# Kernel optimization log

Hardware: AMD Instinct MI355X
Metric: run time of the kernel (lower is better)

Reference implementation:

```python
import jax, jax.numpy as jnp
import numpy as np

EMBED_DIM = 768
NUM_HEADS = 12
SEGMENT_LENGTHS = (2048, 4096, 8192)
DILATION_RATES = (1, 2, 4)
LN_EPS = 1e-5


def setup_inputs() -> dict:
    rng = jax.random.key(0)
    ks = jax.random.split(rng, 6)
    B, S, E = 2, 8192, EMBED_DIM
    xavier = (2.0 / (E + E)) ** 0.5  # xavier_normal std for square fan-in/out
    return {
        "query": jax.random.normal(ks[0], (B, S, E), jnp.float32),
        "key": jax.random.normal(ks[1], (B, S, E), jnp.float32),
        "value": jax.random.normal(ks[2], (B, S, E), jnp.float32),
        "qkv_w": jax.random.normal(ks[3], (3 * E, E), jnp.float32) * xavier,
        "qkv_b": jnp.zeros((3 * E,), jnp.float32),
        "ln_w": jnp.ones((E,), jnp.float32),
        "ln_b": jnp.zeros((E,), jnp.float32),
        "out_w": jax.random.normal(ks[4], (E, E), jnp.float32) * xavier,
        "out_b": jnp.zeros((E,), jnp.float32),
    }


def _dilated_attention(q, k, v):
    # q,k,v: [b, n, h, d].  Heads are partitioned across the
    # (segment_length, dilation_rate) groups; within each group the sequence
    # is split into segments of length s and subsampled with stride r at
    # offset (i % r); plain softmax attention runs inside each dilated segment.
    b, n, h, d = q.shape
    G = len(SEGMENT_LENGTHS)
    g = h // G
    scale = 1.0 / np.sqrt(d)
    out = jnp.zeros_like(q)
    for i, (s, r) in enumerate(zip(SEGMENT_LENGTHS, DILATION_RATES)):
        off = i % r
        h0, h1 = i * g, (i + 1) * g
        m = n // s
        def seg(x):
            # [b, n, g, d] -> [b, m, s/r, g, d]
            return x[:, :, h0:h1].reshape(b, m, s, g, d)[:, :, off::r]
        qi, ki, vi = seg(q), seg(k), seg(v)
        scores = jnp.einsum("bmqgd,bmkgd->bmgqk", qi, ki) * scale
        p = jax.nn.softmax(scores, axis=-1)
        xi = jnp.einsum("bmgqk,bmkgd->bmqgd", p, vi)
        seg_out = jnp.zeros((b, m, s, g, d), q.dtype).at[:, :, off::r].set(xi)
        out = out.at[:, :, h0:h1].set(seg_out.reshape(b, n, g, d))
    return out / G


def reference(query, key, value, qkv_w, qkv_b, ln_w, ln_b, out_w, out_b):
    B, S, E = query.shape
    H = NUM_HEADS
    d = E // H
    # fused QKV projection (cross-attention path of the fused projection)
    q = (query @ qkv_w[:E].T + qkv_b[:E]).reshape(B, S, H, d)
    k = (key @ qkv_w[E:2 * E].T + qkv_b[E:2 * E]).reshape(B, S, H, d)
    v = (value @ qkv_w[2 * E:].T + qkv_b[2 * E:]).reshape(B, S, H, d)
    x = _dilated_attention(q, k, v).reshape(B, S, E)
    # MAGNETO layer norm before output projection
    mu = jnp.mean(x, axis=-1, keepdims=True)
    var = jnp.mean(jnp.square(x - mu), axis=-1, keepdims=True)
    x = (x - mu) * jax.lax.rsqrt(var + LN_EPS) * ln_w + ln_b
    return x @ out_w.T + out_b
```

## Files before the change

### kernel.cpp

```cpp
#include <hip/hip_runtime.h>
#include <hip/hip_bf16.h>
#include <math.h>

typedef __bf16 bf16_t;
typedef __bf16 bf16x8 __attribute__((ext_vector_type(8)));
typedef __bf16 bf16x4 __attribute__((ext_vector_type(4)));
typedef float f32x4 __attribute__((ext_vector_type(4)));

__device__ __forceinline__ void async_ld16(const void* g, void* l) {
  __builtin_amdgcn_global_load_lds(
      (const __attribute__((address_space(1))) unsigned int*)g,
      (__attribute__((address_space(3))) unsigned int*)l, 16, 0, 0);
}

#define BATCH 2
#define SEQ   8192
#define EMB   768
#define NHEAD 12
#define HD    64
#define TOK   (BATCH*SEQ)
#define GATH_PER_B 57344

__device__ __forceinline__ int headoff(int h) {
  int g = h >> 2;
  int base = (g == 0) ? 0 : ((g == 1) ? 32768 : 49152);
  return base + (h & 3) * (8192 >> g);
}

__device__ __forceinline__ float fast_exp2(float x) {
#if __has_builtin(__builtin_amdgcn_exp2f)
  return __builtin_amdgcn_exp2f(x);
#else
  return exp2f(x);
#endif
}

__global__ void k_cast(const float* __restrict__ in, bf16_t* __restrict__ out, int n) {
  int i = (blockIdx.x * blockDim.x + threadIdx.x) * 8;
  if (i < n) {
    float4 a = *(const float4*)(in + i);
    float4 b = *(const float4*)(in + i + 4);
    __attribute__((aligned(16))) bf16_t o[8] = {
        (bf16_t)a.x, (bf16_t)a.y, (bf16_t)a.z, (bf16_t)a.w,
        (bf16_t)b.x, (bf16_t)b.y, (bf16_t)b.z, (bf16_t)b.w};
    *(uint4*)(out + i) = *(uint4*)o;
  }
}

__global__ __launch_bounds__(256, 2)
void k_gemm_qkv(const bf16_t* __restrict__ qb, const bf16_t* __restrict__ kb,
                const bf16_t* __restrict__ vb, const bf16_t* __restrict__ wqkv,
                const float* __restrict__ qkv_bias,
                bf16_t* __restrict__ Qg, bf16_t* __restrict__ Kg, bf16_t* __restrict__ Vb) {
  const int N = 768, K = 768;
  int id = blockIdx.x;
  int wid = (id & 7) * 288 + (id >> 3);
  int z = wid / 768;
  int rem = wid - z * 768;
  int ytile = rem / 6;
  int xtile = rem - ytile * 6;
  int m0 = ytile * 128, n0 = xtile * 128;

  const bf16_t* A = (z == 0) ? qb : (z == 1) ? kb : vb;
  const bf16_t* W = wqkv + (size_t)z * N * K;
  const float* bias = qkv_bias + z * N;

  __shared__ bf16_t As[2][128][32];
  __shared__ bf16_t Bs[2][128][32];

  int tid = threadIdx.x;
  int wave = tid >> 6, lane = tid & 63;
  int q = lane >> 4, c = lane & 15;
  int wm = (wave & 1) * 64, wn = (wave >> 1) * 64;

  auto stage = [&](int k0, int bsel) {
#pragma unroll
    for (int it = 0; it < 2; ++it) {
      int ch = tid + it * 256;
      int row = ch >> 2, kb8 = (ch & 3) << 3;
      async_ld16(A + (size_t)(m0 + row) * K + k0 + kb8, &As[bsel][row][kb8]);
      async_ld16(W + (size_t)(n0 + row) * K + k0 + kb8, &Bs[bsel][row][kb8]);
    }
  };

  f32x4 acc[4][4];
#pragma unroll
  for (int i = 0; i < 4; i++)
#pragma unroll
    for (int j = 0; j < 4; j++) acc[i][j] = (f32x4){0.f, 0.f, 0.f, 0.f};

  stage(0, 0);
#pragma unroll 2
  for (int kt = 0; kt < 24; ++kt) {
    int cur = kt & 1;
    __syncthreads();
    if (kt + 1 < 24) stage((kt + 1) * 32, cur ^ 1);
    bf16x8 af[4], bfr[4];
#pragma unroll
    for (int mi = 0; mi < 4; mi++) af[mi] = *(const bf16x8*)&As[cur][wm + mi * 16 + c][q * 8];
#pragma unroll
    for (int nj = 0; nj < 4; nj++) bfr[nj] = *(const bf16x8*)&Bs[cur][wn + nj * 16 + c][q * 8];
#pragma unroll
    for (int mi = 0; mi < 4; mi++)
#pragma unroll
      for (int nj = 0; nj < 4; nj++)
        acc[mi][nj] = __builtin_amdgcn_mfma_f32_16x16x32_bf16(af[mi], bfr[nj], acc[mi][nj], 0, 0, 0);
  }

  if (z == 2) {
#pragma unroll
    for (int mi = 0; mi < 4; mi++)
#pragma unroll
      for (int nj = 0; nj < 4; nj++)
#pragma unroll
        for (int rg = 0; rg < 4; rg++) {
          int row = m0 + wm + mi * 16 + q * 4 + rg;
          int col = n0 + wn + nj * 16 + c;
          Vb[(size_t)row * N + col] = (bf16_t)(acc[mi][nj][rg] + bias[col]);
        }
  } else {
    bf16_t* dst = (z == 0) ? Qg : Kg;
    float qscale = (z == 0) ? 0.125f * 1.44269504088896f : 1.0f;
#pragma unroll
    for (int mi = 0; mi < 4; mi++)
#pragma unroll
      for (int nj = 0; nj < 4; nj++) {
        int e = n0 + wn + nj * 16 + c;
        int h = e >> 6, dim = e & 63, g2 = h >> 2;
        int rm1 = (1 << g2) - 1, sh = 11 + g2;
        int smask = (2048 << g2) - 1;
        int ho = headoff(h);
#pragma unroll
        for (int rg = 0; rg < 4; rg++) {
          int row = m0 + wm + mi * 16 + q * 4 + rg;
          float v = (acc[mi][nj][rg] + bias[e]) * qscale;
          int bb = row >> 13, p = row & 8191;
          int t = (p & smask) - g2;
          if (t >= 0 && (t & rm1) == 0) {
            int jj = (p >> sh) * 2048 + (t >> g2);
            dst[(size_t)(bb * GATH_PER_B + ho + jj) * HD + dim] = (bf16_t)v;
          }
        }
      }
  }
}

__global__ __launch_bounds__(256, 2)
void k_gemm_out(const bf16_t* __restrict__ A, const bf16_t* __restrict__ W,
                const float* __restrict__ bias, float* __restrict__ C) {
  const int N = 768, K = 768;
  int id = blockIdx.x;
  int wid = (id & 7) * 96 + (id >> 3);
  int ytile = wid / 6;
  int xtile = wid - ytile * 6;
  int m0 = ytile * 128, n0 = xtile * 128;

  __shared__ bf16_t As[2][128][32];
  __shared__ bf16_t Bs[2][128][32];

  int tid = threadIdx.x;
  int wave = tid >> 6, lane = tid & 63;
  int q = lane >> 4, c = lane & 15;
  int wm = (wave & 1) * 64, wn = (wave >> 1) * 64;

  auto stage = [&](int k0, int bsel) {
#pragma unroll
    for (int it = 0; it < 2; ++it) {
      int ch = tid + it * 256;
      int row = ch >> 2, kb8 = (ch & 3) << 3;
      async_ld16(A + (size_t)(m0 + row) * K + k0 + kb8, &As[bsel][row][kb8]);
      async_ld16(W + (size_t)(n0 + row) * K + k0 + kb8, &Bs[bsel][row][kb8]);
    }
  };

  f32x4 acc[4][4];
#pragma unroll
  for (int i = 0; i < 4; i++)
#pragma unroll
    for (int j = 0; j < 4; j++) acc[i][j] = (f32x4){0.f, 0.f, 0.f, 0.f};

  stage(0, 0);
#pragma unroll 2
  for (int kt = 0; kt < 24; ++kt) {
    int cur = kt & 1;
    __syncthreads();
    if (kt + 1 < 24) stage((kt + 1) * 32, cur ^ 1);
    bf16x8 af[4], bfr[4];
#pragma unroll
    for (int mi = 0; mi < 4; mi++) af[mi] = *(const bf16x8*)&As[cur][wm + mi * 16 + c][q * 8];
#pragma unroll
    for (int nj = 0; nj < 4; nj++) bfr[nj] = *(const bf16x8*)&Bs[cur][wn + nj * 16 + c][q * 8];
#pragma unroll
    for (int mi = 0; mi < 4; mi++)
#pragma unroll
      for (int nj = 0; nj < 4; nj++)
        acc[mi][nj] = __builtin_amdgcn_mfma_f32_16x16x32_bf16(af[mi], bfr[nj], acc[mi][nj], 0, 0, 0);
  }
#pragma unroll
  for (int mi = 0; mi < 4; mi++)
#pragma unroll
    for (int nj = 0; nj < 4; nj++)
#pragma unroll
      for (int rg = 0; rg < 4; rg++) {
        int row = m0 + wm + mi * 16 + q * 4 + rg;
        int col = n0 + wn + nj * 16 + c;
        C[(size_t)row * N + col] = acc[mi][nj][rg] + bias[col];
      }
}

__global__ __launch_bounds__(256)
void k_gather_v(const bf16_t* __restrict__ Vb, bf16_t* __restrict__ Vt) {
  int h = blockIdx.y, b = blockIdx.z;
  int g = h >> 2;
  int L = 8192 >> g;
  int jj0 = blockIdx.x * 64;
  if (jj0 >= L) return;
  int s = 2048 << g;
  int hb = b * GATH_PER_B + headoff(h);
  int tid = threadIdx.x;

  __shared__ bf16_t tile[64][72];

#pragma unroll
  for (int it = 0; it < 2; ++it) {
    int ch = tid + it * 256;
    int rowl = ch >> 3, db = (ch & 7) << 3;
    int jj = jj0 + rowl;
    int p = (jj >> 11) * s + g + ((jj & 2047) << g);
    *(uint4*)&tile[rowl][db] = *(const uint4*)(Vb + ((size_t)(b * SEQ + p)) * EMB + h * HD + db);
  }
  __syncthreads();
  int dim = tid >> 2, sub = tid & 3;
  __attribute__((aligned(16))) bf16_t tmp[16];
#pragma unroll
  for (int sl = 0; sl < 16; sl++) {
    int t = sub * 16 + sl;
    int pos = (t & 3) * 16 + (t >> 2);
    tmp[sl] = tile[pos][dim];
  }
  size_t vdst = ((size_t)hb) * HD + (size_t)dim * L + jj0 + sub * 16;
  *(uint4*)(Vt + vdst) = *(uint4*)&tmp[0];
  *(uint4*)(Vt + vdst + 8) = *(uint4*)&tmp[8];
}

__global__ __launch_bounds__(256, 2)
void k_attn(const bf16_t* __restrict__ Qg, const bf16_t* __restrict__ Kg,
            const bf16_t* __restrict__ Vt, bf16_t* __restrict__ xattn) {
  int u = blockIdx.x;
  int seg = u % 56, qt = u / 56;
  int b = seg / 28, t = seg % 28;
  int g, h, si;
  if (t < 16)      { g = 0; h = t >> 2;              si = t & 3; }
  else if (t < 24) { g = 1; h = 4 + ((t - 16) >> 1); si = (t - 16) & 1; }
  else             { g = 2; h = 8 + (t - 24);        si = 0; }
  int L = 8192 >> g, s = 2048 << g;
  int hb = b * GATH_PER_B + headoff(h);
  int jj0 = si * 2048 + qt * 128;
  int kvbase = si * 2048;

  __shared__ bf16_t Ps[128][64];
  __shared__ bf16_t Ks[2][128][64];
  __shared__ bf16_t Vs[2][64][128];

  int tid = threadIdx.x, wave = tid >> 6, lane = tid & 63;
  int q = lane >> 4, c = lane & 15;
  int cx = c & 7;
  int wm = wave * 32;

  auto stageK = [&](int kt, int bsel) {
#pragma unroll
    for (int it = 0; it < 4; ++it) {
      int ch = tid + it * 256;
      int row = ch >> 3, pc = ch & 7, lc = pc ^ (row & 7);
      async_ld16(Kg + ((size_t)(hb + kvbase + kt * 128 + row)) * HD + lc * 8,
                 &Ks[bsel][0][0] + ch * 8);
    }
  };
  auto stageV = [&](int kt, int bsel) {
#pragma unroll
    for (int it = 0; it < 4; ++it) {
      int ch = tid + it * 256;
      int dim = ch >> 4, pc = ch & 15, lc = pc ^ (dim & 7);
      async_ld16(Vt + ((size_t)hb) * HD + (size_t)dim * L + kvbase + kt * 128 + lc * 8,
                 &Vs[bsel][0][0] + ch * 8);
    }
  };

  bf16_t* Qs = &Ps[0][0];
#pragma unroll
  for (int it = 0; it < 4; ++it) {
    int ch = tid + it * 256;
    int row = ch >> 3, pc = ch & 7, lc = pc ^ (row & 7);
    async_ld16(Qg + ((size_t)(hb + jj0 + row)) * HD + lc * 8, Qs + ch * 8);
  }
  stageK(0, 0);
  stageV(0, 0);
  __syncthreads();

  bf16x8 aq[2][2];
#pragma unroll
  for (int mi = 0; mi < 2; mi++)
#pragma unroll
    for (int kq = 0; kq < 2; kq++) {
      int pch = (kq * 4 + q) ^ cx;
      aq[mi][kq] = *(const bf16x8*)(Qs + (size_t)(wm + mi * 16 + c) * HD + pch * 8);
    }

  float lrow[2][4];
  f32x4 O[2][4];
#pragma unroll
  for (int mi = 0; mi < 2; mi++)
#pragma unroll
    for (int rg = 0; rg < 4; rg++) lrow[mi][rg] = 0.f;
#pragma unroll
  for (int mi = 0; mi < 2; mi++)
#pragma unroll
    for (int vd = 0; vd < 4; vd++) O[mi][vd] = (f32x4){0.f, 0.f, 0.f, 0.f};

#pragma unroll 2
  for (int kt = 0; kt < 16; ++kt) {
    int cur = kt & 1;
    if (kt < 15) {
      stageK(kt + 1, cur ^ 1);
      stageV(kt + 1, cur ^ 1);
    }

    f32x4 Sv[2][8];
#pragma unroll
    for (int mi = 0; mi < 2; mi++)
#pragma unroll
      for (int nj = 0; nj < 8; nj++) Sv[mi][nj] = (f32x4){0.f, 0.f, 0.f, 0.f};
#pragma unroll
    for (int kq = 0; kq < 2; kq++) {
      int pch = (kq * 4 + q) ^ cx;
      bf16x8 bk[8];
#pragma unroll
      for (int nj = 0; nj < 8; nj++) bk[nj] = *(const bf16x8*)&Ks[cur][nj * 16 + c][pch * 8];
#pragma unroll
      for (int mi = 0; mi < 2; mi++)
#pragma unroll
        for (int nj = 0; nj < 8; nj++)
          Sv[mi][nj] = __builtin_amdgcn_mfma_f32_16x16x32_bf16(aq[mi][kq], bk[nj], Sv[mi][nj], 0, 0, 0);
    }

#pragma unroll
    for (int half = 0; half < 2; ++half) {
#pragma unroll
      for (int mi = 0; mi < 2; mi++)
#pragma unroll
        for (int rg = 0; rg < 4; rg++) {
          bf16x4 p4;
          float rs = 0.f;
#pragma unroll
          for (int j = 0; j < 4; j++) {
            float p = fast_exp2(Sv[mi][half * 4 + j][rg]);
            rs += p;
            p4[j] = (bf16_t)p;
          }
          lrow[mi][rg] += rs;
          int row = wm + mi * 16 + q * 4 + rg;
          int u8 = c ^ ((row & 7) << 1);
          *(bf16x4*)((char*)&Ps[row][0] + u8 * 8) = p4;
        }
#pragma unroll
      for (int kk2 = 0; kk2 < 2; ++kk2) {
        bf16x8 ap[2], bv[4];
#pragma unroll
        for (int mi = 0; mi < 2; mi++) {
          int u8 = (kk2 * 8 + q * 2) ^ (cx << 1);
          ap[mi] = *(const bf16x8*)((char*)&Ps[wm + mi * 16 + c][0] + u8 * 8);
        }
#pragma unroll
        for (int vd = 0; vd < 4; vd++) {
          int pch = (half * 8 + kk2 * 4 + q) ^ cx;
          bv[vd] = *(const bf16x8*)&Vs[cur][vd * 16 + c][pch * 8];
        }
#pragma unroll
        for (int mi = 0; mi < 2; mi++)
#pragma unroll
          for (int vd = 0; vd < 4; vd++)
            O[mi][vd] = __builtin_amdgcn_mfma_f32_16x16x32_bf16(ap[mi], bv[vd], O[mi][vd], 0, 0, 0);
      }
    }
    __syncthreads();
  }

  const float inv3 = 1.0f / 3.0f;
#pragma unroll
  for (int mi = 0; mi < 2; mi++)
#pragma unroll
    for (int rg = 0; rg < 4; rg++) {
      float l = lrow[mi][rg];
#pragma unroll
      for (int d = 1; d < 16; d <<= 1) l += __shfl_xor(l, d, 64);
      float invl = inv3 / l;
      int jj = jj0 + wm + mi * 16 + q * 4 + rg;
      int p = si * s + g + ((jj & 2047) << g);
      size_t base = ((size_t)(b * SEQ + p)) * EMB + h * HD;
#pragma unroll
      for (int vd = 0; vd < 4; vd++)
        xattn[base + vd * 16 + c] = (bf16_t)(O[mi][vd][rg] * invl);
    }
}

__global__ __launch_bounds__(256)
void k_ln(const bf16_t* __restrict__ x, const float* __restrict__ lnw,
          const float* __restrict__ lnb, bf16_t* __restrict__ y) {
  int wave = threadIdx.x >> 6, lane = threadIdx.x & 63;
  int row = blockIdx.x * 4 + wave;
  const bf16_t* xr = x + (size_t)row * EMB + lane * 12;
  bf16x4 v4[3];
#pragma unroll
  for (int j = 0; j < 3; j++) v4[j] = *(const bf16x4*)(xr + j * 4);
  float v[12], s = 0.f, s2 = 0.f;
#pragma unroll
  for (int j = 0; j < 12; j++) {
    v[j] = (float)v4[j >> 2][j & 3];
    s += v[j];
    s2 += v[j] * v[j];
  }
#pragma unroll
  for (int d = 1; d < 64; d <<= 1) { s += __shfl_xor(s, d, 64); s2 += __shfl_xor(s2, d, 64); }
  float mu = s * (1.f / 768.f);
  float var = s2 * (1.f / 768.f) - mu * mu;
  float rstd = rsqrtf(var + 1e-5f);
  const float4* wr = (const float4*)(lnw + lane * 12);
  const float4* br = (const float4*)(lnb + lane * 12);
  bf16_t* yr = y + (size_t)row * EMB + lane * 12;
#pragma unroll
  for (int j = 0; j < 3; j++) {
    float4 w = wr[j], bb = br[j];
    bf16x4 o;
    o[0] = (bf16_t)((v[j * 4 + 0] - mu) * rstd * w.x + bb.x);
    o[1] = (bf16_t)((v[j * 4 + 1] - mu) * rstd * w.y + bb.y);
    o[2] = (bf16_t)((v[j * 4 + 2] - mu) * rstd * w.z + bb.z);
    o[3] = (bf16_t)((v[j * 4 + 3] - mu) * rstd * w.w + bb.w);
    *(bf16x4*)(yr + j * 4) = o;
  }
}

extern "C" void kernel_launch(void* const* d_in, const int* in_sizes, int n_in,
                              void* d_out, int out_size, void* d_ws, size_t ws_size,
                              hipStream_t stream) {
  const float* query = (const float*)d_in[0];
  const float* key   = (const float*)d_in[1];
  const float* value = (const float*)d_in[2];
  const float* qkv_w = (const float*)d_in[3];
  const float* qkv_b = (const float*)d_in[4];
  const float* ln_w  = (const float*)d_in[5];
  const float* ln_b  = (const float*)d_in[6];
  const float* out_w = (const float*)d_in[7];
  const float* out_b = (const float*)d_in[8];
  float* out = (float*)d_out;

  char* ws = (char*)d_ws;
  const size_t A = (size_t)TOK * EMB * 2;
  bf16_t* qb    = (bf16_t*)(ws + 0 * A);
  bf16_t* kb    = (bf16_t*)(ws + 1 * A);
  bf16_t* vb    = (bf16_t*)(ws + 2 * A);
  bf16_t* Vb    = (bf16_t*)(ws + 3 * A);
  bf16_t* Qg    = (bf16_t*)(ws + 4 * A);
  bf16_t* Kg    = (bf16_t*)(ws + 5 * A);
  bf16_t* wqkv  = (bf16_t*)(ws + 6 * A);
  bf16_t* wout  = (bf16_t*)(ws + 6 * A + (size_t)2304 * 768 * 2);
  bf16_t* Vt    = vb;
  bf16_t* xattn = qb;
  bf16_t* xnorm = kb;

  k_cast<<<6144, 256, 0, stream>>>(query, qb, TOK * EMB);
  k_cast<<<6144, 256, 0, stream>>>(key,   kb, TOK * EMB);
  k_cast<<<6144, 256, 0, stream>>>(value, vb, TOK * EMB);
  k_cast<<<864, 256, 0, stream>>>(qkv_w, wqkv, 2304 * 768);
  k_cast<<<288, 256, 0, stream>>>(out_w, wout, 768 * 768);

  k_gemm_qkv<<<2304, 256, 0, stream>>>(qb, kb, vb, wqkv, qkv_b, Qg, Kg, Vb);

  dim3 gg(128, 12, 2);
  k_gather_v<<<gg, 256, 0, stream>>>(Vb, Vt);

  hipMemsetAsync(xattn, 0, A, stream);
  k_attn<<<896, 256, 0, stream>>>(Qg, Kg, Vt, xattn);

  k_ln<<<4096, 256, 0, stream>>>(xattn, ln_w, ln_b, xnorm);

  k_gemm_out<<<768, 256, 0, stream>>>(xnorm, wout, out_b, out);
}
```

Baseline: 418.0 us.

## Fuse fp32-to-bf16 activation cast into QKV GEMM operand loading

```diff
diff --git a/kernel.cpp b/kernel.cpp
--- a/kernel.cpp
+++ b/kernel.cpp
@@ -47,9 +47,9 @@
   }
 }
 
-__global__ __launch_bounds__(256, 2)
-void k_gemm_qkv(const bf16_t* __restrict__ qb, const bf16_t* __restrict__ kb,
-                const bf16_t* __restrict__ vb, const bf16_t* __restrict__ wqkv,
+__global__ __launch_bounds__(256, 3)
+void k_gemm_qkv(const float* __restrict__ qf, const float* __restrict__ kf,
+                const float* __restrict__ vf, const bf16_t* __restrict__ wqkv,
                 const float* __restrict__ qkv_bias,
                 bf16_t* __restrict__ Qg, bf16_t* __restrict__ Kg, bf16_t* __restrict__ Vb) {
   const int N = 768, K = 768;
@@ -61,24 +61,31 @@
   int xtile = rem - ytile * 6;
   int m0 = ytile * 128, n0 = xtile * 128;
 
-  const bf16_t* A = (z == 0) ? qb : (z == 1) ? kb : vb;
+  const float* A = (z == 0) ? qf : (z == 1) ? kf : vf;
   const bf16_t* W = wqkv + (size_t)z * N * K;
   const float* bias = qkv_bias + z * N;
 
-  __shared__ bf16_t As[2][128][32];
+  __shared__ float  As[2][128][32];
   __shared__ bf16_t Bs[2][128][32];
 
   int tid = threadIdx.x;
   int wave = tid >> 6, lane = tid & 63;
   int q = lane >> 4, c = lane & 15;
+  int cx = c & 7;
   int wm = (wave & 1) * 64, wn = (wave >> 1) * 64;
 
   auto stage = [&](int k0, int bsel) {
+#pragma unroll
+    for (int it = 0; it < 4; ++it) {
+      int ch = tid + it * 256;
+      int row = ch >> 3, pc = ch & 7, lc = pc ^ (row & 7);
+      async_ld16(A + (size_t)(m0 + row) * K + k0 + lc * 4,
+                 (float*)&As[bsel][0][0] + ch * 4);
+    }
 #pragma unroll
     for (int it = 0; it < 2; ++it) {
       int ch = tid + it * 256;
       int row = ch >> 2, kb8 = (ch & 3) << 3;
-      async_ld16(A + (size_t)(m0 + row) * K + k0 + kb8, &As[bsel][row][kb8]);
       async_ld16(W + (size_t)(n0 + row) * K + k0 + kb8, &Bs[bsel][row][kb8]);
     }
   };
@@ -88,6 +95,8 @@
   for (int i = 0; i < 4; i++)
 #pragma unroll
     for (int j = 0; j < 4; j++) acc[i][j] = (f32x4){0.f, 0.f, 0.f, 0.f};
+
+  int s0 = (q * 2) ^ cx, s1 = (q * 2 + 1) ^ cx;
 
   stage(0, 0);
 #pragma unroll 2
@@ -97,7 +106,15 @@
     if (kt + 1 < 24) stage((kt + 1) * 32, cur ^ 1);
     bf16x8 af[4], bfr[4];
 #pragma unroll
-    for (int mi = 0; mi < 4; mi++) af[mi] = *(const bf16x8*)&As[cur][wm + mi * 16 + c][q * 8];
+    for (int mi = 0; mi < 4; mi++) {
+      const float* ar = &As[cur][wm + mi * 16 + c][0];
+      f32x4 a0 = *(const f32x4*)(ar + s0 * 4);
+      f32x4 a1 = *(const f32x4*)(ar + s1 * 4);
+      bf16x8 t;
+#pragma unroll
+      for (int j = 0; j < 4; j++) { t[j] = (bf16_t)a0[j]; t[4 + j] = (bf16_t)a1[j]; }
+      af[mi] = t;
+    }
 #pragma unroll
     for (int nj = 0; nj < 4; nj++) bfr[nj] = *(const bf16x8*)&Bs[cur][wn + nj * 16 + c][q * 8];
 #pragma unroll
@@ -145,7 +162,7 @@
   }
 }
 
-__global__ __launch_bounds__(256, 2)
+__global__ __launch_bounds__(256, 4)
 void k_gemm_out(const bf16_t* __restrict__ A, const bf16_t* __restrict__ W,
                 const float* __restrict__ bias, float* __restrict__ C) {
   const int N = 768, K = 768;
@@ -455,25 +472,19 @@
 
   char* ws = (char*)d_ws;
   const size_t A = (size_t)TOK * EMB * 2;
-  bf16_t* qb    = (bf16_t*)(ws + 0 * A);
-  bf16_t* kb    = (bf16_t*)(ws + 1 * A);
-  bf16_t* vb    = (bf16_t*)(ws + 2 * A);
+  bf16_t* xattn = (bf16_t*)(ws + 0 * A);
+  bf16_t* xnorm = (bf16_t*)(ws + 1 * A);
+  bf16_t* Vt    = (bf16_t*)(ws + 2 * A);
   bf16_t* Vb    = (bf16_t*)(ws + 3 * A);
   bf16_t* Qg    = (bf16_t*)(ws + 4 * A);
   bf16_t* Kg    = (bf16_t*)(ws + 5 * A);
   bf16_t* wqkv  = (bf16_t*)(ws + 6 * A);
   bf16_t* wout  = (bf16_t*)(ws + 6 * A + (size_t)2304 * 768 * 2);
-  bf16_t* Vt    = vb;
-  bf16_t* xattn = qb;
-  bf16_t* xnorm = kb;
-
-  k_cast<<<6144, 256, 0, stream>>>(query, qb, TOK * EMB);
-  k_cast<<<6144, 256, 0, stream>>>(key,   kb, TOK * EMB);
-  k_cast<<<6144, 256, 0, stream>>>(value, vb, TOK * EMB);
+
   k_cast<<<864, 256, 0, stream>>>(qkv_w, wqkv, 2304 * 768);
   k_cast<<<288, 256, 0, stream>>>(out_w, wout, 768 * 768);
 
-  k_gemm_qkv<<<2304, 256, 0, stream>>>(qb, kb, vb, wqkv, qkv_b, Qg, Kg, Vb);
+  k_gemm_qkv<<<2304, 256, 0, stream>>>(query, key, value, wqkv, qkv_b, Qg, Kg, Vb);
 
   dim3 gg(128, 12, 2);
   k_gather_v<<<gg, 256, 0, stream>>>(Vb, Vt);
```

Result: slower. 433.8 us (+3.8%).
